# Performance work log

Hardware: AMD Instinct MI355X
Metric: run time of the kernel (lower is better)

Reference implementation:

```python
import jax, jax.numpy as jnp
import numpy as np

NUM_EXPERTS = 8
HIDDEN = 1024
INTERMEDIATE = 2816
TOTAL_TOKENS = 4096  # 512 tokens per expert


def setup_inputs() -> dict:
    key = jax.random.key(0)
    k_x, k1, k2, k3 = jax.random.split(key, 4)
    hiddens = jax.random.normal(k_x, (TOTAL_TOKENS, HIDDEN), dtype=jnp.float32)
    # tokens assumed pre-sorted by expert; equal-sized groups here
    batch_sizes = jnp.full((NUM_EXPERTS,), TOTAL_TOKENS // NUM_EXPERTS, dtype=jnp.int64)
    w1_weight = jax.random.normal(k1, (NUM_EXPERTS, HIDDEN, INTERMEDIATE), dtype=jnp.float32)
    w2_weight = jax.random.normal(k2, (NUM_EXPERTS, INTERMEDIATE, HIDDEN), dtype=jnp.float32)
    w3_weight = jax.random.normal(k3, (NUM_EXPERTS, HIDDEN, INTERMEDIATE), dtype=jnp.float32)
    return {
        "hiddens": hiddens,
        "w1_weight": w1_weight,
        "w2_weight": w2_weight,
        "w3_weight": w3_weight,
        "batch_sizes": batch_sizes,
    }


def _grouped_moe(hiddens, w1, w2, w3, batch_sizes):
    """Grouped SwiGLU FFN: tokens are contiguous per expert (sizes = batch_sizes).

    Jit-safe formulation: map each token to its expert id, then run one masked
    dense GEMM trio per expert (small fixed expert count). Zero rows contribute
    exactly zero (silu(0)*0 == 0), so no final masking of the output is needed.
    """
    num_experts = w1.shape[0]
    total_tokens = hiddens.shape[0]
    bounds = jnp.cumsum(batch_sizes)  # [E] exclusive-right boundaries
    expert_ids = jnp.searchsorted(bounds, jnp.arange(total_tokens), side="right")  # [T]
    out = jnp.zeros((total_tokens, w2.shape[-1]), dtype=hiddens.dtype)
    for e in range(num_experts):
        mask = (expert_ids == e)[:, None]  # [T, 1]
        xe = jnp.where(mask, hiddens, 0)   # zero out other experts' tokens
        up = jax.nn.silu(xe @ w1[e]) * (xe @ w3[e])  # [T, F] SwiGLU
        out = out + up @ w2[e]             # [T, H]
    return out


def reference(hiddens, w1_weight, w2_weight, w3_weight, batch_sizes):
    return _grouped_moe(hiddens, w1_weight, w2_weight, w3_weight, batch_sizes)
```

## Files before the change

### kernel.cpp

```cpp
#include <hip/hip_runtime.h>
#include <hip/hip_bf16.h>

#define NE 8
#define HD 1024
#define ID 2816
#define TT 4096
#define BM 128
#define BK 32
#define BN1 128
#define BN2 64
#define MAXMT (TT / BM + NE)

typedef __attribute__((ext_vector_type(4))) float f32x4;
typedef __attribute__((ext_vector_type(8))) short s16x8;

__device__ __forceinline__ unsigned int f2bfpk(float lo, float hi) {
  float2 t; t.x = lo; t.y = hi;
  union { __hip_bfloat162 h2; unsigned int u; } cv;
  cv.h2 = __float22bfloat162_rn(t);
  return cv.u;
}

__device__ __forceinline__ void lds_barrier() {
  asm volatile("s_waitcnt lgkmcnt(0)" ::: "memory");
  __builtin_amdgcn_s_barrier();
}

__device__ __forceinline__ bool map_tile(const void* bsp, int mt, int& e,
                                         int& mstart, int& rowend) {
  const int* w = (const int*)bsp;
  bool is64 = (w[1] == 0) && (w[3] == 0) && (w[5] == 0) && (w[7] == 0) &&
              ((w[0] | w[2] | w[4] | w[6]) != 0);
  long long start = 0;
  int rem = mt;
  for (int i = 0; i < NE; ++i) {
    long long b = is64 ? ((const long long*)bsp)[i] : (long long)w[i];
    if (b < 0) b = 0;
    int tiles = (int)((b + BM - 1) / BM);
    if (rem < tiles) {
      long long m0 = start + (long long)rem * BM;
      long long me = start + b;
      if (m0 >= TT) return false;
      if (me > TT) me = TT;
      e = i; mstart = (int)m0; rowend = (int)me;
      return true;
    }
    rem -= tiles;
    start += b;
  }
  return false;
}

__global__ __launch_bounds__(256) void cvt_x(const float* __restrict__ x,
                                             __hip_bfloat16* __restrict__ xb) {
  size_t i = ((size_t)blockIdx.x * 256 + threadIdx.x) * 8;
  f32x4 v0 = *(const f32x4*)(x + i);
  f32x4 v1 = *(const f32x4*)(x + i + 4);
  s16x8 o;
  unsigned int p0 = f2bfpk(v0[0], v0[1]), p1 = f2bfpk(v0[2], v0[3]);
  unsigned int p2 = f2bfpk(v1[0], v1[1]), p3 = f2bfpk(v1[2], v1[3]);
  o[0] = (short)(p0 & 0xffff); o[1] = (short)(p0 >> 16);
  o[2] = (short)(p1 & 0xffff); o[3] = (short)(p1 >> 16);
  o[4] = (short)(p2 & 0xffff); o[5] = (short)(p2 >> 16);
  o[6] = (short)(p3 & 0xffff); o[7] = (short)(p3 >> 16);
  *(s16x8*)((unsigned short*)xb + i) = o;
}

__global__ __launch_bounds__(512, 2) void moe_gemm1(
    const __hip_bfloat16* __restrict__ xbf, const float* __restrict__ w1,
    const float* __restrict__ w3, const void* __restrict__ bsp,
    __hip_bfloat16* __restrict__ up) {
  __shared__ __align__(16) char As[2][BM * 80];
  __shared__ __align__(16) char B1s[2][BN1 * 80];
  __shared__ __align__(16) char B3s[2][BN1 * 80];

  const int NWG = (ID / BN1) * MAXMT;
  int bid = blockIdx.x;
  int logical = (bid & 7) * (NWG >> 3) + (bid >> 3);
  int mt = logical % MAXMT;
  int nt = logical / MAXMT;
  int e, mstart, rowend;
  if (!map_tile(bsp, mt, e, mstart, rowend)) return;
  const int n0 = nt * BN1;
  const int tid = threadIdx.x;

  const int lane = tid & 63;
  const int wv = tid >> 6;
  const int wr = wv >> 2, wc = wv & 3;
  const int q = lane >> 4, r16 = lane & 15;

  const int a_k8 = (tid & 3) * 8;
  const int a_r0 = tid >> 2;
  const int b_n = tid & 127;
  const int b_kq = tid >> 7;

  const bool ok0 = (mstart + a_r0) < rowend;

  const __hip_bfloat16* xc = xbf + (size_t)(mstart + a_r0) * HD + a_k8;
  const float* w1c = w1 + (size_t)e * HD * ID + (size_t)(4 * b_kq) * ID + n0 + b_n;
  const float* w3c = w3 + (size_t)e * HD * ID + (size_t)(4 * b_kq) * ID + n0 + b_n;

  f32x4 acc1[4][2], acc3[4][2];
#pragma unroll
  for (int i = 0; i < 4; ++i)
#pragma unroll
    for (int j = 0; j < 2; ++j) { acc1[i][j] = (f32x4)0.f; acc3[i][j] = (f32x4)0.f; }

  s16x8 A0, A1;
  float W1a[2][4], W3a[2][4], W1b[2][4], W3b[2][4];

  auto load_t = [&](s16x8& A, float (*W1_)[4], float (*W3_)[4]) {
    A = ok0 ? *(const s16x8*)xc : (s16x8)0;
    xc += BK;
#pragma unroll
    for (int g = 0; g < 2; ++g)
#pragma unroll
      for (int kk = 0; kk < 4; ++kk) {
        W1_[g][kk] = w1c[(size_t)(g * 16 + kk) * ID];
        W3_[g][kk] = w3c[(size_t)(g * 16 + kk) * ID];
      }
    w1c += (size_t)BK * ID; w3c += (size_t)BK * ID;
  };
  auto store_t = [&](char* As_, char* B1_, char* B3_, const s16x8& A,
                     const float (*W1_)[4], const float (*W3_)[4]) {
    *(s16x8*)(As_ + a_r0 * 80 + a_k8 * 2) = A;
#pragma unroll
    for (int g = 0; g < 2; ++g) {
      unsigned long long p1 =
          (unsigned long long)f2bfpk(W1_[g][0], W1_[g][1]) |
          ((unsigned long long)f2bfpk(W1_[g][2], W1_[g][3]) << 32);
      *(unsigned long long*)(B1_ + b_n * 80 + b_kq * 8 + g * 32) = p1;
      unsigned long long p3 =
          (unsigned long long)f2bfpk(W3_[g][0], W3_[g][1]) |
          ((unsigned long long)f2bfpk(W3_[g][2], W3_[g][3]) << 32);
      *(unsigned long long*)(B3_ + b_n * 80 + b_kq * 8 + g * 32) = p3;
    }
  };
  auto compute_t = [&](const char* As_, const char* B1_, const char* B3_) {
    s16x8 a[4], b1[2], b3[2];
#pragma unroll
    for (int i = 0; i < 4; ++i)
      a[i] = *(const s16x8*)(As_ + (wr * 64 + i * 16 + r16) * 80 + q * 16);
#pragma unroll
    for (int j = 0; j < 2; ++j) {
      b1[j] = *(const s16x8*)(B1_ + (wc * 32 + j * 16 + r16) * 80 + q * 16);
      b3[j] = *(const s16x8*)(B3_ + (wc * 32 + j * 16 + r16) * 80 + q * 16);
    }
#pragma unroll
    for (int i = 0; i < 4; ++i)
#pragma unroll
      for (int j = 0; j < 2; ++j) {
        acc1[i][j] = __builtin_amdgcn_mfma_f32_16x16x32_bf16(a[i], b1[j], acc1[i][j], 0, 0, 0);
        acc3[i][j] = __builtin_amdgcn_mfma_f32_16x16x32_bf16(a[i], b3[j], acc3[i][j], 0, 0, 0);
      }
  };

  const int NK = HD / BK;
  load_t(A0, W1a, W3a);
  load_t(A1, W1b, W3b);
  store_t(As[0], B1s[0], B3s[0], A0, W1a, W3a);
  lds_barrier();
  for (int kt = 0; kt < NK; kt += 2) {
    if (kt + 2 < NK) load_t(A0, W1a, W3a);
    compute_t(As[0], B1s[0], B3s[0]);
    store_t(As[1], B1s[1], B3s[1], A1, W1b, W3b);
    lds_barrier();
    if (kt + 3 < NK) load_t(A1, W1b, W3b);
    compute_t(As[1], B1s[1], B3s[1]);
    if (kt + 2 < NK) {
      store_t(As[0], B1s[0], B3s[0], A0, W1a, W3a);
      lds_barrier();
    }
  }

#pragma unroll
  for (int i = 0; i < 4; ++i)
#pragma unroll
    for (int r = 0; r < 4; ++r) {
      int gm = mstart + wr * 64 + i * 16 + q * 4 + r;
      if (gm < rowend) {
#pragma unroll
        for (int j = 0; j < 2; ++j) {
          float v1 = acc1[i][j][r], v3 = acc3[i][j][r];
          float s = v1 / (1.f + __expf(-v1));
          up[(size_t)gm * ID + n0 + wc * 32 + j * 16 + r16] = __float2bfloat16(s * v3);
        }
      }
    }
}

__global__ __launch_bounds__(256, 4) void moe_gemm2(
    const __hip_bfloat16* __restrict__ up, const float* __restrict__ w2,
    const void* __restrict__ bsp, float* __restrict__ out) {
  __shared__ __align__(16) char As[2][BM * 80];
  __shared__ __align__(16) char Bs[2][BN2 * 80];

  const int NWG = (HD / BN2) * MAXMT;
  int bid = blockIdx.x;
  int logical = (bid & 7) * (NWG >> 3) + (bid >> 3);
  int mt = logical % MAXMT;
  int nt = logical / MAXMT;
  int e, mstart, rowend;
  if (!map_tile(bsp, mt, e, mstart, rowend)) return;
  const int n0 = nt * BN2;
  const int tid = threadIdx.x;

  const int lane = tid & 63;
  const int wv = tid >> 6;
  const int wr = wv >> 1, wc = wv & 1;
  const int q = lane >> 4, r16 = lane & 15;

  const int a_k8 = (tid & 3) * 8;
  const int a_r0 = tid >> 2;
  const int b_n = tid & 63;
  const int b_kq = tid >> 6;

  const bool ok0 = (mstart + a_r0) < rowend;
  const bool ok1 = (mstart + a_r0 + 64) < rowend;

  const __hip_bfloat16* uc = up + (size_t)(mstart + a_r0) * ID + a_k8;
  const float* w2c = w2 + (size_t)e * ID * HD + (size_t)(4 * b_kq) * HD + n0 + b_n;

  f32x4 acc[4][2];
#pragma unroll
  for (int i = 0; i < 4; ++i)
#pragma unroll
    for (int j = 0; j < 2; ++j) acc[i][j] = (f32x4)0.f;

  s16x8 A0[2], A1[2];
  float Wa[2][4], Wb[2][4];

  auto load_t = [&](s16x8* A, float (*W_)[4]) {
    A[0] = ok0 ? *(const s16x8*)uc : (s16x8)0;
    A[1] = ok1 ? *(const s16x8*)(uc + (size_t)64 * ID) : (s16x8)0;
    uc += BK;
#pragma unroll
    for (int g = 0; g < 2; ++g)
#pragma unroll
      for (int kk = 0; kk < 4; ++kk)
        W_[g][kk] = w2c[(size_t)(g * 16 + kk) * HD];
    w2c += (size_t)BK * HD;
  };
  auto store_t = [&](char* As_, char* B_, const s16x8* A, const float (*W_)[4]) {
    *(s16x8*)(As_ + a_r0 * 80 + a_k8 * 2) = A[0];
    *(s16x8*)(As_ + (a_r0 + 64) * 80 + a_k8 * 2) = A[1];
#pragma unroll
    for (int g = 0; g < 2; ++g) {
      unsigned long long p =
          (unsigned long long)f2bfpk(W_[g][0], W_[g][1]) |
          ((unsigned long long)f2bfpk(W_[g][2], W_[g][3]) << 32);
      *(unsigned long long*)(B_ + b_n * 80 + b_kq * 8 + g * 32) = p;
    }
  };
  auto compute_t = [&](const char* As_, const char* B_) {
    s16x8 a[4], b[2];
#pragma unroll
    for (int i = 0; i < 4; ++i)
      a[i] = *(const s16x8*)(As_ + (wr * 64 + i * 16 + r16) * 80 + q * 16);
#pragma unroll
    for (int j = 0; j < 2; ++j)
      b[j] = *(const s16x8*)(B_ + (wc * 32 + j * 16 + r16) * 80 + q * 16);
#pragma unroll
    for (int i = 0; i < 4; ++i)
#pragma unroll
      for (int j = 0; j < 2; ++j)
        acc[i][j] = __builtin_amdgcn_mfma_f32_16x16x32_bf16(a[i], b[j], acc[i][j], 0, 0, 0);
  };

  const int NK = ID / BK;
  load_t(A0, Wa);
  load_t(A1, Wb);
  store_t(As[0], Bs[0], A0, Wa);
  lds_barrier();
  for (int kt = 0; kt < NK; kt += 2) {
    if (kt + 2 < NK) load_t(A0, Wa);
    compute_t(As[0], Bs[0]);
    store_t(As[1], Bs[1], A1, Wb);
    lds_barrier();
    if (kt + 3 < NK) load_t(A1, Wb);
    compute_t(As[1], Bs[1]);
    if (kt + 2 < NK) {
      store_t(As[0], Bs[0], A0, Wa);
      lds_barrier();
    }
  }

#pragma unroll
  for (int i = 0; i < 4; ++i)
#pragma unroll
    for (int r = 0; r < 4; ++r) {
      int gm = mstart + wr * 64 + i * 16 + q * 4 + r;
      if (gm < rowend) {
#pragma unroll
        for (int j = 0; j < 2; ++j)
          out[(size_t)gm * HD + n0 + wc * 32 + j * 16 + r16] = acc[i][j][r];
      }
    }
}

extern "C" void kernel_launch(void* const* d_in, const int* in_sizes, int n_in,
                              void* d_out, int out_size, void* d_ws, size_t ws_size,
                              hipStream_t stream) {
  const float* x = (const float*)d_in[0];
  const float* w1 = (const float*)d_in[1];
  const float* w2 = (const float*)d_in[2];
  const float* w3 = (const float*)d_in[3];
  const void* bs = d_in[4];
  float* out = (float*)d_out;
  __hip_bfloat16* xbf = (__hip_bfloat16*)d_ws;
  __hip_bfloat16* up = (__hip_bfloat16*)((char*)d_ws + (size_t)TT * HD * 2);

  hipMemsetAsync(d_out, 0, (size_t)out_size * sizeof(float), stream);

  cvt_x<<<dim3(TT * HD / (8 * 256)), dim3(256), 0, stream>>>(x, xbf);
  moe_gemm1<<<dim3((ID / BN1) * MAXMT), dim3(512), 0, stream>>>(xbf, w1, w3, bs, up);
  moe_gemm2<<<dim3((HD / BN2) * MAXMT), dim3(256), 0, stream>>>(up, w2, bs, out);
}
```

Before: 219.0 us.

## Pre-tile activations into MFMA fragment layout and stream them via direct-to-LDS loads

The conversion kernel now writes bf16 activations pre-tiled per M-tile and K-slice in MFMA fragment order. GEMM1 fetches those tiles with global_load_lds straight into a 4-deep LDS ring, skipping register staging. GEMM1 also drops to 256 threads with a 64-wide N tile. Both GEMMs switch the weight LDS layout to fragment order, so each thread writes one 16-byte store per k-slice. The intent is to cut register-to-LDS traffic and bank conflicts and improve latency hiding, at the cost of more workgroups and re-reading X across twice as many N tiles.

Result: faster. 184.9 us (-15.6%).

```diff
diff --git a/kernel.cpp b/kernel.cpp
--- a/kernel.cpp
+++ b/kernel.cpp
@@ -7,12 +7,16 @@
 #define TT 4096
 #define BM 128
 #define BK 32
-#define BN1 128
+#define BN1 64
 #define BN2 64
 #define MAXMT (TT / BM + NE)
+#define NKS1 (HD / BK)
+#define NKS2 (ID / BK)
+#define ATILE 8192
 
 typedef __attribute__((ext_vector_type(4))) float f32x4;
 typedef __attribute__((ext_vector_type(8))) short s16x8;
+typedef __attribute__((ext_vector_type(4))) int i32x4;
 
 __device__ __forceinline__ unsigned int f2bfpk(float lo, float hi) {
   float2 t; t.x = lo; t.y = hi;
@@ -24,6 +28,12 @@
 __device__ __forceinline__ void lds_barrier() {
   asm volatile("s_waitcnt lgkmcnt(0)" ::: "memory");
   __builtin_amdgcn_s_barrier();
+}
+
+__device__ __forceinline__ void glds16(const void* g, void* l) {
+  __builtin_amdgcn_global_load_lds(
+      (const __attribute__((address_space(1))) void*)g,
+      (__attribute__((address_space(3))) void*)l, 16, 0, 0);
 }
 
 __device__ __forceinline__ bool map_tile(const void* bsp, int mt, int& e,
@@ -51,28 +61,44 @@
   return false;
 }
 
-__global__ __launch_bounds__(256) void cvt_x(const float* __restrict__ x,
-                                             __hip_bfloat16* __restrict__ xb) {
-  size_t i = ((size_t)blockIdx.x * 256 + threadIdx.x) * 8;
-  f32x4 v0 = *(const f32x4*)(x + i);
-  f32x4 v1 = *(const f32x4*)(x + i + 4);
-  s16x8 o;
-  unsigned int p0 = f2bfpk(v0[0], v0[1]), p1 = f2bfpk(v0[2], v0[3]);
-  unsigned int p2 = f2bfpk(v1[0], v1[1]), p3 = f2bfpk(v1[2], v1[3]);
-  o[0] = (short)(p0 & 0xffff); o[1] = (short)(p0 >> 16);
-  o[2] = (short)(p1 & 0xffff); o[3] = (short)(p1 >> 16);
-  o[4] = (short)(p2 & 0xffff); o[5] = (short)(p2 >> 16);
-  o[6] = (short)(p3 & 0xffff); o[7] = (short)(p3 >> 16);
-  *(s16x8*)((unsigned short*)xb + i) = o;
-}
-
-__global__ __launch_bounds__(512, 2) void moe_gemm1(
-    const __hip_bfloat16* __restrict__ xbf, const float* __restrict__ w1,
+__global__ __launch_bounds__(256) void cvt_xt(const float* __restrict__ x,
+                                              const void* __restrict__ bsp,
+                                              unsigned short* __restrict__ xt) {
+  int mt = blockIdx.x >> 5;
+  int ks = blockIdx.x & 31;
+  int e, mstart, rowend;
+  if (!map_tile(bsp, mt, e, mstart, rowend)) return;
+  int t = threadIdx.x;
+  int lane = t & 63;
+  int r = lane & 15, q = lane >> 4;
+  unsigned short* ob = xt + ((size_t)mt * NKS1 + ks) * (ATILE / 2);
+#pragma unroll
+  for (int h = 0; h < 2; ++h) {
+    int f = h * 4 + (t >> 6);
+    int row = mstart + f * 16 + r;
+    s16x8 o = (s16x8)0;
+    if (row < rowend) {
+      const float* src = x + (size_t)row * HD + ks * 32 + q * 8;
+      f32x4 v0 = *(const f32x4*)src;
+      f32x4 v1 = *(const f32x4*)(src + 4);
+      unsigned int d0 = f2bfpk(v0[0], v0[1]), d1 = f2bfpk(v0[2], v0[3]);
+      unsigned int d2 = f2bfpk(v1[0], v1[1]), d3 = f2bfpk(v1[2], v1[3]);
+      o[0] = (short)d0; o[1] = (short)(d0 >> 16);
+      o[2] = (short)d1; o[3] = (short)(d1 >> 16);
+      o[4] = (short)d2; o[5] = (short)(d2 >> 16);
+      o[6] = (short)d3; o[7] = (short)(d3 >> 16);
+    }
+    *(s16x8*)(ob + h * 2048 + t * 8) = o;
+  }
+}
+
+__global__ __launch_bounds__(256, 3) void moe_gemm1(
+    const unsigned short* __restrict__ xt, const float* __restrict__ w1,
     const float* __restrict__ w3, const void* __restrict__ bsp,
     __hip_bfloat16* __restrict__ up) {
-  __shared__ __align__(16) char As[2][BM * 80];
-  __shared__ __align__(16) char B1s[2][BN1 * 80];
-  __shared__ __align__(16) char B3s[2][BN1 * 80];
+  __shared__ __align__(16) char As[4][ATILE];
+  __shared__ __align__(16) char B1s[2][4096];
+  __shared__ __align__(16) char B3s[2][4096];
 
   const int NWG = (ID / BN1) * MAXMT;
   int bid = blockIdx.x;
@@ -83,22 +109,16 @@
   if (!map_tile(bsp, mt, e, mstart, rowend)) return;
   const int n0 = nt * BN1;
   const int tid = threadIdx.x;
-
   const int lane = tid & 63;
   const int wv = tid >> 6;
-  const int wr = wv >> 2, wc = wv & 3;
+  const int wr = wv >> 1, wc = wv & 1;
   const int q = lane >> 4, r16 = lane & 15;
 
-  const int a_k8 = (tid & 3) * 8;
-  const int a_r0 = tid >> 2;
-  const int b_n = tid & 127;
-  const int b_kq = tid >> 7;
-
-  const bool ok0 = (mstart + a_r0) < rowend;
-
-  const __hip_bfloat16* xc = xbf + (size_t)(mstart + a_r0) * HD + a_k8;
-  const float* w1c = w1 + (size_t)e * HD * ID + (size_t)(4 * b_kq) * ID + n0 + b_n;
-  const float* w3c = w3 + (size_t)e * HD * ID + (size_t)(4 * b_kq) * ID + n0 + b_n;
+  const int b_n = tid & 63, b_kq = tid >> 6;
+  const int boff = (b_n >> 4) * 1024 + b_kq * 256 + (b_n & 15) * 16;
+  const char* agp = (const char*)xt + (size_t)mt * NKS1 * ATILE + tid * 16;
+  const float* w1c = w1 + (size_t)e * HD * ID + (size_t)(8 * b_kq) * ID + n0 + b_n;
+  const float* w3c = w3 + (size_t)e * HD * ID + (size_t)(8 * b_kq) * ID + n0 + b_n;
 
   f32x4 acc1[4][2], acc3[4][2];
 #pragma unroll
@@ -106,45 +126,40 @@
 #pragma unroll
     for (int j = 0; j < 2; ++j) { acc1[i][j] = (f32x4)0.f; acc3[i][j] = (f32x4)0.f; }
 
-  s16x8 A0, A1;
-  float W1a[2][4], W3a[2][4], W1b[2][4], W3b[2][4];
-
-  auto load_t = [&](s16x8& A, float (*W1_)[4], float (*W3_)[4]) {
-    A = ok0 ? *(const s16x8*)xc : (s16x8)0;
-    xc += BK;
-#pragma unroll
-    for (int g = 0; g < 2; ++g)
-#pragma unroll
-      for (int kk = 0; kk < 4; ++kk) {
-        W1_[g][kk] = w1c[(size_t)(g * 16 + kk) * ID];
-        W3_[g][kk] = w3c[(size_t)(g * 16 + kk) * ID];
-      }
+  float Wa1[8], Wa3[8], Wb1[8], Wb3[8];
+
+  auto gldsA = [&](int k, int buf) {
+    const char* s = agp + (size_t)k * ATILE;
+    char* d = &As[buf][0] + tid * 16;
+    glds16(s, d);
+    glds16(s + 4096, d + 4096);
+  };
+  auto loadB = [&](float* W1_, float* W3_) {
+#pragma unroll
+    for (int i = 0; i < 8; ++i) {
+      W1_[i] = w1c[(size_t)i * ID];
+      W3_[i] = w3c[(size_t)i * ID];
+    }
     w1c += (size_t)BK * ID; w3c += (size_t)BK * ID;
   };
-  auto store_t = [&](char* As_, char* B1_, char* B3_, const s16x8& A,
-                     const float (*W1_)[4], const float (*W3_)[4]) {
-    *(s16x8*)(As_ + a_r0 * 80 + a_k8 * 2) = A;
-#pragma unroll
-    for (int g = 0; g < 2; ++g) {
-      unsigned long long p1 =
-          (unsigned long long)f2bfpk(W1_[g][0], W1_[g][1]) |
-          ((unsigned long long)f2bfpk(W1_[g][2], W1_[g][3]) << 32);
-      *(unsigned long long*)(B1_ + b_n * 80 + b_kq * 8 + g * 32) = p1;
-      unsigned long long p3 =
-          (unsigned long long)f2bfpk(W3_[g][0], W3_[g][1]) |
-          ((unsigned long long)f2bfpk(W3_[g][2], W3_[g][3]) << 32);
-      *(unsigned long long*)(B3_ + b_n * 80 + b_kq * 8 + g * 32) = p3;
-    }
-  };
-  auto compute_t = [&](const char* As_, const char* B1_, const char* B3_) {
+  auto storeB = [&](int buf, const float* W1_, const float* W3_) {
+    i32x4 p1, p3;
+    p1[0] = (int)f2bfpk(W1_[0], W1_[1]); p1[1] = (int)f2bfpk(W1_[2], W1_[3]);
+    p1[2] = (int)f2bfpk(W1_[4], W1_[5]); p1[3] = (int)f2bfpk(W1_[6], W1_[7]);
+    *(i32x4*)(B1s[buf] + boff) = p1;
+    p3[0] = (int)f2bfpk(W3_[0], W3_[1]); p3[1] = (int)f2bfpk(W3_[2], W3_[3]);
+    p3[2] = (int)f2bfpk(W3_[4], W3_[5]); p3[3] = (int)f2bfpk(W3_[6], W3_[7]);
+    *(i32x4*)(B3s[buf] + boff) = p3;
+  };
+  auto compute = [&](int ab, int bb) {
     s16x8 a[4], b1[2], b3[2];
 #pragma unroll
     for (int i = 0; i < 4; ++i)
-      a[i] = *(const s16x8*)(As_ + (wr * 64 + i * 16 + r16) * 80 + q * 16);
+      a[i] = *(const s16x8*)(As[ab] + (wr * 4 + i) * 1024 + lane * 16);
 #pragma unroll
     for (int j = 0; j < 2; ++j) {
-      b1[j] = *(const s16x8*)(B1_ + (wc * 32 + j * 16 + r16) * 80 + q * 16);
-      b3[j] = *(const s16x8*)(B3_ + (wc * 32 + j * 16 + r16) * 80 + q * 16);
+      b1[j] = *(const s16x8*)(B1s[bb] + (wc * 2 + j) * 1024 + lane * 16);
+      b3[j] = *(const s16x8*)(B3s[bb] + (wc * 2 + j) * 1024 + lane * 16);
     }
 #pragma unroll
     for (int i = 0; i < 4; ++i)
@@ -155,23 +170,32 @@
       }
   };
 
-  const int NK = HD / BK;
-  load_t(A0, W1a, W3a);
-  load_t(A1, W1b, W3b);
-  store_t(As[0], B1s[0], B3s[0], A0, W1a, W3a);
+#define G1PHASE(AB, GD, BB, SB, LW1, LW3, SW1, SW3, KC)    \
+  if (kt + (KC) + 2 < NKS1) {                              \
+    gldsA(kt + (KC) + 2, (GD));                            \
+    __builtin_amdgcn_sched_barrier(0);                     \
+    loadB(LW1, LW3);                                       \
+  }                                                        \
+  compute((AB), (BB));                                     \
+  if (kt + (KC) + 1 < NKS1) {                              \
+    storeB((SB), SW1, SW3);                                \
+    lds_barrier();                                         \
+  }
+
+  gldsA(0, 0); gldsA(1, 1);
+  __builtin_amdgcn_sched_barrier(0);
+  loadB(Wa1, Wa3);
+  loadB(Wb1, Wb3);
+  storeB(0, Wa1, Wa3);
   lds_barrier();
-  for (int kt = 0; kt < NK; kt += 2) {
-    if (kt + 2 < NK) load_t(A0, W1a, W3a);
-    compute_t(As[0], B1s[0], B3s[0]);
-    store_t(As[1], B1s[1], B3s[1], A1, W1b, W3b);
-    lds_barrier();
-    if (kt + 3 < NK) load_t(A1, W1b, W3b);
-    compute_t(As[1], B1s[1], B3s[1]);
-    if (kt + 2 < NK) {
-      store_t(As[0], B1s[0], B3s[0], A0, W1a, W3a);
-      lds_barrier();
-    }
-  }
+
+  for (int kt = 0; kt < NKS1; kt += 4) {
+    G1PHASE(0, 2, 0, 1, Wa1, Wa3, Wb1, Wb3, 0)
+    G1PHASE(1, 3, 1, 0, Wb1, Wb3, Wa1, Wa3, 1)
+    G1PHASE(2, 0, 0, 1, Wa1, Wa3, Wb1, Wb3, 2)
+    G1PHASE(3, 1, 1, 0, Wb1, Wb3, Wa1, Wa3, 3)
+  }
+#undef G1PHASE
 
 #pragma unroll
   for (int i = 0; i < 4; ++i)
@@ -189,11 +213,11 @@
     }
 }
 
-__global__ __launch_bounds__(256, 4) void moe_gemm2(
+__global__ __launch_bounds__(256, 3) void moe_gemm2(
     const __hip_bfloat16* __restrict__ up, const float* __restrict__ w2,
     const void* __restrict__ bsp, float* __restrict__ out) {
   __shared__ __align__(16) char As[2][BM * 80];
-  __shared__ __align__(16) char Bs[2][BN2 * 80];
+  __shared__ __align__(16) char Bs[2][4096];
 
   const int NWG = (HD / BN2) * MAXMT;
   int bid = blockIdx.x;
@@ -204,7 +228,6 @@
   if (!map_tile(bsp, mt, e, mstart, rowend)) return;
   const int n0 = nt * BN2;
   const int tid = threadIdx.x;
-
   const int lane = tid & 63;
   const int wv = tid >> 6;
   const int wr = wv >> 1, wc = wv & 1;
@@ -212,14 +235,14 @@
 
   const int a_k8 = (tid & 3) * 8;
   const int a_r0 = tid >> 2;
-  const int b_n = tid & 63;
-  const int b_kq = tid >> 6;
+  const int b_n = tid & 63, b_kq = tid >> 6;
+  const int boff = (b_n >> 4) * 1024 + b_kq * 256 + (b_n & 15) * 16;
 
   const bool ok0 = (mstart + a_r0) < rowend;
   const bool ok1 = (mstart + a_r0 + 64) < rowend;
 
   const __hip_bfloat16* uc = up + (size_t)(mstart + a_r0) * ID + a_k8;
-  const float* w2c = w2 + (size_t)e * ID * HD + (size_t)(4 * b_kq) * HD + n0 + b_n;
+  const float* w2c = w2 + (size_t)e * ID * HD + (size_t)(8 * b_kq) * HD + n0 + b_n;
 
   f32x4 acc[4][2];
 #pragma unroll
@@ -227,39 +250,33 @@
 #pragma unroll
     for (int j = 0; j < 2; ++j) acc[i][j] = (f32x4)0.f;
 
-  s16x8 A0[2], A1[2];
-  float Wa[2][4], Wb[2][4];
-
-  auto load_t = [&](s16x8* A, float (*W_)[4]) {
+  s16x8 Aa[2], Ab[2];
+  float Wa[8], Wb[8];
+
+  auto loadT = [&](s16x8* A, float* W_) {
     A[0] = ok0 ? *(const s16x8*)uc : (s16x8)0;
     A[1] = ok1 ? *(const s16x8*)(uc + (size_t)64 * ID) : (s16x8)0;
     uc += BK;
 #pragma unroll
-    for (int g = 0; g < 2; ++g)
-#pragma unroll
-      for (int kk = 0; kk < 4; ++kk)
-        W_[g][kk] = w2c[(size_t)(g * 16 + kk) * HD];
+    for (int i = 0; i < 8; ++i) W_[i] = w2c[(size_t)i * HD];
     w2c += (size_t)BK * HD;
   };
-  auto store_t = [&](char* As_, char* B_, const s16x8* A, const float (*W_)[4]) {
-    *(s16x8*)(As_ + a_r0 * 80 + a_k8 * 2) = A[0];
-    *(s16x8*)(As_ + (a_r0 + 64) * 80 + a_k8 * 2) = A[1];
-#pragma unroll
-    for (int g = 0; g < 2; ++g) {
-      unsigned long long p =
-          (unsigned long long)f2bfpk(W_[g][0], W_[g][1]) |
-          ((unsigned long long)f2bfpk(W_[g][2], W_[g][3]) << 32);
-      *(unsigned long long*)(B_ + b_n * 80 + b_kq * 8 + g * 32) = p;
-    }
-  };
-  auto compute_t = [&](const char* As_, const char* B_) {
+  auto storeT = [&](int buf, const s16x8* A, const float* W_) {
+    *(s16x8*)(As[buf] + a_r0 * 80 + a_k8 * 2) = A[0];
+    *(s16x8*)(As[buf] + (a_r0 + 64) * 80 + a_k8 * 2) = A[1];
+    i32x4 p;
+    p[0] = (int)f2bfpk(W_[0], W_[1]); p[1] = (int)f2bfpk(W_[2], W_[3]);
+    p[2] = (int)f2bfpk(W_[4], W_[5]); p[3] = (int)f2bfpk(W_[6], W_[7]);
+    *(i32x4*)(Bs[buf] + boff) = p;
+  };
+  auto compute = [&](int buf) {
     s16x8 a[4], b[2];
 #pragma unroll
     for (int i = 0; i < 4; ++i)
-      a[i] = *(const s16x8*)(As_ + (wr * 64 + i * 16 + r16) * 80 + q * 16);
+      a[i] = *(const s16x8*)(As[buf] + (wr * 64 + i * 16 + r16) * 80 + q * 16);
 #pragma unroll
     for (int j = 0; j < 2; ++j)
-      b[j] = *(const s16x8*)(B_ + (wc * 32 + j * 16 + r16) * 80 + q * 16);
+      b[j] = *(const s16x8*)(Bs[buf] + (wc * 2 + j) * 1024 + lane * 16);
 #pragma unroll
     for (int i = 0; i < 4; ++i)
 #pragma unroll
@@ -267,23 +284,20 @@
         acc[i][j] = __builtin_amdgcn_mfma_f32_16x16x32_bf16(a[i], b[j], acc[i][j], 0, 0, 0);
   };
 
-  const int NK = ID / BK;
-  load_t(A0, Wa);
-  load_t(A1, Wb);
-  store_t(As[0], Bs[0], A0, Wa);
+#define G2PHASE(AB, SB, LA, LW, SA, SW, KC)                 \
+  if (kt + (KC) + 2 < NKS2) { loadT(LA, LW); }              \
+  compute(AB);                                              \
+  if (kt + (KC) + 1 < NKS2) { storeT((SB), SA, SW); lds_barrier(); }
+
+  loadT(Aa, Wa);
+  loadT(Ab, Wb);
+  storeT(0, Aa, Wa);
   lds_barrier();
-  for (int kt = 0; kt < NK; kt += 2) {
-    if (kt + 2 < NK) load_t(A0, Wa);
-    compute_t(As[0], Bs[0]);
-    store_t(As[1], Bs[1], A1, Wb);
-    lds_barrier();
-    if (kt + 3 < NK) load_t(A1, Wb);
-    compute_t(As[1], Bs[1]);
-    if (kt + 2 < NK) {
-      store_t(As[0], Bs[0], A0, Wa);
-      lds_barrier();
-    }
-  }
+  for (int kt = 0; kt < NKS2; kt += 2) {
+    G2PHASE(0, 1, Aa, Wa, Ab, Wb, 0)
+    G2PHASE(1, 0, Ab, Wb, Aa, Wa, 1)
+  }
+#undef G2PHASE
 
 #pragma unroll
   for (int i = 0; i < 4; ++i)
@@ -307,12 +321,13 @@
   const float* w3 = (const float*)d_in[3];
   const void* bs = d_in[4];
   float* out = (float*)d_out;
-  __hip_bfloat16* xbf = (__hip_bfloat16*)d_ws;
-  __hip_bfloat16* up = (__hip_bfloat16*)((char*)d_ws + (size_t)TT * HD * 2);
+  unsigned short* xt = (unsigned short*)d_ws;
+  __hip_bfloat16* up =
+      (__hip_bfloat16*)((char*)d_ws + (size_t)MAXMT * NKS1 * ATILE);
 
   hipMemsetAsync(d_out, 0, (size_t)out_size * sizeof(float), stream);
 
-  cvt_x<<<dim3(TT * HD / (8 * 256)), dim3(256), 0, stream>>>(x, xbf);
-  moe_gemm1<<<dim3((ID / BN1) * MAXMT), dim3(512), 0, stream>>>(xbf, w1, w3, bs, up);
+  cvt_xt<<<dim3(MAXMT * NKS1), dim3(256), 0, stream>>>(x, bs, xt);
+  moe_gemm1<<<dim3((ID / BN1) * MAXMT), dim3(256), 0, stream>>>(xt, w1, w3, bs, up);
   moe_gemm2<<<dim3((HD / BN2) * MAXMT), dim3(256), 0, stream>>>(up, w2, bs, out);
 }
```
